# Performance work log

Hardware: AMD Instinct MI355X
Metric: run time of the kernel (lower is better)

## Reference

```python
import jax, jax.numpy as jnp
import numpy as np

N_NODE, N_USER = 100000, 30000
N_REL, N_BASIS = 8, 30
EMB, OUT = 32, 32
E = 1600000
BATCH = 16384
H1, H2, H3 = 64, 32, 16
NEG_SLOPE = 0.2


def setup_inputs() -> dict:
    key = jax.random.key(0)
    ks = jax.random.split(key, 20)
    g = lambda k, shape: jax.random.normal(k, shape, dtype=jnp.float32) * 0.05
    inp = {
        "x_ids": jnp.arange(N_NODE, dtype=jnp.int64 if jax.config.jax_enable_x64 else jnp.int32),
        "edge_index": jax.random.randint(ks[0], (2, E), 0, N_NODE),
        "edge_type": jax.random.randint(ks[1], (E,), 0, N_REL),
        "users": jax.random.randint(ks[2], (BATCH,), 0, N_USER),
        "bundles": jax.random.randint(ks[3], (BATCH,), 0, N_NODE),
        # parameters
        "emb": g(ks[4], (N_NODE, EMB)),
        "basis": g(ks[5], (N_BASIS, EMB, OUT)),
        "weight": g(ks[6], (N_REL, N_BASIS)),
        "att": g(ks[7], (N_REL, 2 * OUT)),
        "root": g(ks[8], (EMB, OUT)),
        "bias": jnp.zeros((OUT,), jnp.float32),
        "W1": g(ks[9], (2 * OUT, H1)), "b1": jnp.zeros((H1,), jnp.float32),
        "W2": g(ks[10], (H1, H2)), "b2": jnp.zeros((H2,), jnp.float32),
        "W3": g(ks[11], (H2, H3)), "b3": jnp.zeros((H3,), jnp.float32),
        "Wo": g(ks[12], (H3, 1)), "bo": jnp.zeros((1,), jnp.float32),
    }
    return inp


def _tgcn_fwd(x_ids, edge_index, edge_type, users, bundles,
              emb, basis, weight, att, root, bias,
              W1, b1, W2, b2, W3, b3, Wo, bo):
    N = emb.shape[0]
    R = weight.shape[0]
    O = basis.shape[2]
    x = emb[x_ids]                                   # (N, F) embedding lookup
    # basis decomposition: (R, F, O)
    w = (weight @ basis.reshape(N_BASIS, -1)).reshape(R, EMB, O)
    # transform every node under every relation once, then gather per edge
    xh = jnp.einsum('nf,rfo->nro', x, w)             # (N, R, O)
    src, dst = edge_index[0], edge_index[1]          # j (source), i (target)
    h_i = xh[dst, edge_type]                         # (E, O)
    h_j = xh[src, edge_type]                         # (E, O)
    a = att[edge_type]                               # (E, 2O)
    alpha = (h_i * a[:, :O]).sum(-1) + (h_j * a[:, O:]).sum(-1)
    alpha = jax.nn.leaky_relu(alpha, NEG_SLOPE)
    # segment softmax keyed by (target node, relation)
    seg_key = dst * R + edge_type
    n_seg = N * R
    amax = jax.ops.segment_max(alpha, seg_key, num_segments=n_seg)
    ex = jnp.exp(alpha - amax[seg_key])
    denom = jax.ops.segment_sum(ex, seg_key, num_segments=n_seg)
    alpha = ex / (denom[seg_key] + 1e-16)
    # scatter-add weighted messages into target nodes
    agg = jax.ops.segment_sum(h_j * alpha[:, None], dst, num_segments=N)
    h = jax.nn.relu(agg + x @ root + bias)           # update + ReLU
    z = jnp.concatenate([h[users], h[bundles]], axis=1)  # (B, 2O)
    z = jax.nn.relu(z @ W1 + b1)
    z = jax.nn.relu(z @ W2 + b2)
    z = jax.nn.relu(z @ W3 + b3)
    return z @ Wo + bo                               # (B, 1) logits


def reference(x_ids, edge_index, edge_type, users, bundles,
              emb, basis, weight, att, root, bias,
              W1, b1, W2, b2, W3, b3, Wo, bo):
    return _tgcn_fwd(x_ids, edge_index, edge_type, users, bundles,
                     emb, basis, weight, att, root, bias,
                     W1, b1, W2, b2, W3, b3, Wo, bo)
```

## Files before the change

### kernel.cpp

```cpp
#include <hip/hip_runtime.h>
#include <hip/hip_bf16.h>

#define N_NODE 100000
#define N_REL  8
#define EMB    32
#define OUT    32
#define N_BASIS 30
#define E_EDGE 1600000
#define BATCH  16384
#define H1 64
#define H2 32
#define H3 16
#define NEG_SLOPE 0.2f

#define BSH   9
#define NBKT  196
#define BCAP  12288
#define PCH   8192

__global__ __launch_bounds__(256) void k0_basis(const float* __restrict__ weight,
                                                const float* __restrict__ basis,
                                                float* __restrict__ w) {
    int i = blockIdx.x * 256 + threadIdx.x;
    if (i >= N_REL * EMB * OUT) return;
    int r = i >> 10, fo = i & 1023;
    float acc = 0.f;
    #pragma unroll
    for (int b = 0; b < N_BASIS; b++)
        acc = fmaf(weight[r * N_BASIS + b], basis[b * (EMB * OUT) + fo], acc);
    w[i] = acc;
}

__global__ __launch_bounds__(256) void k0b_wa(const float* __restrict__ w,
                                              const float* __restrict__ att,
                                              float* __restrict__ wa) {
    int i = blockIdx.x * 256 + threadIdx.x;
    if (i >= 512) return;
    int which = i >> 8, rf = i & 255, r = rf >> 5, f = rf & 31;
    const float* wrow = w + (r * 32 + f) * 32;
    const float* arow = att + r * 64 + which * 32;
    float acc = 0.f;
    #pragma unroll
    for (int o = 0; o < 32; o++) acc = fmaf(wrow[o], arow[o], acc);
    wa[i] = acc;
}

__global__ __launch_bounds__(256, 4) void k1_transform(const int* __restrict__ x_ids,
                                                       const float* __restrict__ emb,
                                                       const float* __restrict__ w,
                                                       unsigned short* __restrict__ xh) {
    const int t = threadIdx.x;
    const int o = t & 31;
    const int r = t >> 5;

    float wc[EMB];
    #pragma unroll
    for (int f = 0; f < EMB; f++) wc[f] = w[(r * EMB + f) * OUT + o];

    for (int n0 = blockIdx.x * 4; n0 < N_NODE; n0 += gridDim.x * 4) {
        const float* __restrict__ x0 =
            emb + (size_t)__builtin_amdgcn_readfirstlane(x_ids[n0 + 0]) * EMB;
        const float* __restrict__ x1 =
            emb + (size_t)__builtin_amdgcn_readfirstlane(x_ids[n0 + 1]) * EMB;
        const float* __restrict__ x2 =
            emb + (size_t)__builtin_amdgcn_readfirstlane(x_ids[n0 + 2]) * EMB;
        const float* __restrict__ x3 =
            emb + (size_t)__builtin_amdgcn_readfirstlane(x_ids[n0 + 3]) * EMB;

        float a0 = 0.f, a1 = 0.f, a2 = 0.f, a3 = 0.f;
        #pragma unroll
        for (int f = 0; f < EMB; f++) {
            a0 = fmaf(x0[f], wc[f], a0);
            a1 = fmaf(x1[f], wc[f], a1);
            a2 = fmaf(x2[f], wc[f], a2);
            a3 = fmaf(x3[f], wc[f], a3);
        }
        __hip_bfloat16 b0 = __float2bfloat16(a0);
        __hip_bfloat16 b1 = __float2bfloat16(a1);
        __hip_bfloat16 b2 = __float2bfloat16(a2);
        __hip_bfloat16 b3 = __float2bfloat16(a3);
        xh[(size_t)(n0 + 0) * 256 + t] = *(unsigned short*)&b0;
        xh[(size_t)(n0 + 1) * 256 + t] = *(unsigned short*)&b1;
        xh[(size_t)(n0 + 2) * 256 + t] = *(unsigned short*)&b2;
        xh[(size_t)(n0 + 3) * 256 + t] = *(unsigned short*)&b3;
    }
}

__global__ __launch_bounds__(256) void k_p(const int* __restrict__ x_ids,
                                           const float* __restrict__ emb,
                                           const float* __restrict__ wa,
                                           float* __restrict__ p_i,
                                           float* __restrict__ p_j) {
    __shared__ float wis[256], wjs[256];
    int t = threadIdx.x;
    for (int i = t; i < 512; i += 256) {
        int which = i >> 8, r = (i >> 5) & 7, f = i & 31;
        float v = wa[i];
        if (which == 0) wis[f * 8 + r] = v; else wjs[f * 8 + r] = v;
    }
    __syncthreads();
    int tg = blockIdx.x * 256 + t;
    int n = tg >> 3, r = tg & 7;
    int id = x_ids[n];
    const float4* xr = (const float4*)(emb + (size_t)id * EMB);
    float ai = 0.f, aj = 0.f;
    #pragma unroll
    for (int c = 0; c < 8; c++) {
        float4 xv = xr[c];
        ai = fmaf(xv.x, wis[(4 * c + 0) * 8 + r], ai);
        aj = fmaf(xv.x, wjs[(4 * c + 0) * 8 + r], aj);
        ai = fmaf(xv.y, wis[(4 * c + 1) * 8 + r], ai);
        aj = fmaf(xv.y, wjs[(4 * c + 1) * 8 + r], aj);
        ai = fmaf(xv.z, wis[(4 * c + 2) * 8 + r], ai);
        aj = fmaf(xv.z, wjs[(4 * c + 2) * 8 + r], aj);
        ai = fmaf(xv.w, wis[(4 * c + 3) * 8 + r], ai);
        aj = fmaf(xv.w, wjs[(4 * c + 3) * 8 + r], aj);
    }
    p_i[tg] = ai;
    p_j[tg] = aj;
}

__global__ __launch_bounds__(256) void k_init(const int* __restrict__ x_ids,
                                              const float* __restrict__ emb,
                                              const float* __restrict__ root,
                                              const float* __restrict__ bias,
                                              float* __restrict__ agg) {
    __shared__ float rs[EMB * OUT];
    __shared__ float bs[OUT];
    int t = threadIdx.x;
    for (int i = t; i < EMB * OUT; i += 256) rs[i] = root[i];
    if (t < OUT) bs[t] = bias[t];
    __syncthreads();
    int tg = blockIdx.x * 256 + t;
    int n = tg >> 5, o = tg & 31;
    int id = x_ids[n];
    const float* xr = emb + (size_t)id * EMB;
    float a = bs[o];
    #pragma unroll
    for (int f = 0; f < EMB; f++) a = fmaf(xr[f], rs[f * 32 + o], a);
    agg[tg] = a;
}

__global__ __launch_bounds__(256) void k_bhist(const int* __restrict__ dst,
                                               unsigned* __restrict__ bcnt) {
    __shared__ unsigned h[NBKT];
    int t = threadIdx.x;
    for (int i = t; i < NBKT; i += 256) h[i] = 0;
    __syncthreads();
    int beg = blockIdx.x * PCH, end = min(beg + PCH, E_EDGE);
    for (int e = beg + t; e < end; e += 256)
        atomicAdd(&h[(unsigned)dst[e] >> BSH], 1u);
    __syncthreads();
    for (int i = t; i < NBKT; i += 256)
        if (h[i]) atomicAdd(&bcnt[i], h[i]);
}

__global__ __launch_bounds__(256) void k_bscan(const unsigned* __restrict__ bcnt,
                                               unsigned* __restrict__ bbase,
                                               unsigned* __restrict__ bcursor) {
    __shared__ unsigned s[256];
    int t = threadIdx.x;
    unsigned v = (t < NBKT) ? bcnt[t] : 0u;
    s[t] = v;
    __syncthreads();
    for (int off = 1; off < 256; off <<= 1) {
        unsigned y = (t >= off) ? s[t - off] : 0u;
        __syncthreads();
        s[t] += y;
        __syncthreads();
    }
    unsigned ex = s[t] - v;
    if (t < NBKT) { bbase[t] = ex; bcursor[t] = ex; }
    if (t == 0) bbase[NBKT] = E_EDGE;
}

__global__ __launch_bounds__(256) void k_part(const int* __restrict__ src,
                                              const int* __restrict__ dst,
                                              const int* __restrict__ et,
                                              unsigned* __restrict__ bcursor,
                                              unsigned* __restrict__ part) {
    __shared__ unsigned long long stage[PCH];
    __shared__ unsigned hist[NBKT], lbase[NBKT], lcur[NBKT], gbase[NBKT];
    __shared__ unsigned sc[256];
    int t = threadIdx.x;
    for (int i = t; i < NBKT; i += 256) hist[i] = 0;
    __syncthreads();
    int beg = blockIdx.x * PCH, end = min(beg + PCH, E_EDGE);
    int n = end - beg;
    for (int e = beg + t; e < end; e += 256)
        atomicAdd(&hist[(unsigned)dst[e] >> BSH], 1u);
    __syncthreads();
    unsigned v = (t < NBKT) ? hist[t] : 0u;
    sc[t] = v;
    __syncthreads();
    for (int off = 1; off < 256; off <<= 1) {
        unsigned y = (t >= off) ? sc[t - off] : 0u;
        __syncthreads();
        sc[t] += y;
        __syncthreads();
    }
    if (t < NBKT) { lbase[t] = sc[t] - v; lcur[t] = sc[t] - v; }
    __syncthreads();
    for (int e = beg + t; e < end; e += 256) {
        int d = dst[e];
        unsigned b = (unsigned)d >> BSH;
        unsigned ent = ((unsigned)(d & 511) << 20)
                     | ((unsigned)src[e] << 3) | (unsigned)et[e];
        unsigned pos = atomicAdd(&lcur[b], 1u);
        stage[pos] = ((unsigned long long)b << 32) | ent;
    }
    __syncthreads();
    if (t < NBKT && hist[t]) gbase[t] = atomicAdd(&bcursor[t], hist[t]);
    __syncthreads();
    for (int i = t; i < n; i += 256) {
        unsigned long long s64 = stage[i];
        unsigned b = (unsigned)(s64 >> 32);
        unsigned ent = (unsigned)s64;
        part[gbase[b] + (i - lbase[b])] = ent;
    }
}

__global__ __launch_bounds__(256) void k_sort(const unsigned* __restrict__ bbase,
                                              const unsigned* __restrict__ part,
                                              int* __restrict__ payload,
                                              int* __restrict__ basep) {
    __shared__ unsigned ent[BCAP];
    __shared__ unsigned ent2[BCAP];
    __shared__ unsigned hist[512], dbase[512], dcur[512];
    __shared__ unsigned sc[256];
    int t = threadIdx.x;
    int b = blockIdx.x;
    unsigned s0 = bbase[b], s1 = bbase[b + 1];
    int n = (int)(s1 - s0);
    if (n > BCAP) n = BCAP;
    for (int i = t; i < 512; i += 256) hist[i] = 0;
    __syncthreads();
    for (int i = t; i < n; i += 256) {
        unsigned e = part[s0 + i];
        ent[i] = e;
        atomicAdd(&hist[e >> 20], 1u);
    }
    __syncthreads();
    unsigned v0 = hist[2 * t], v1 = hist[2 * t + 1];
    unsigned s = v0 + v1;
    sc[t] = s;
    __syncthreads();
    for (int off = 1; off < 256; off <<= 1) {
        unsigned y = (t >= off) ? sc[t - off] : 0u;
        __syncthreads();
        sc[t] += y;
        __syncthreads();
    }
    unsigned ex = sc[t] - s;
    dbase[2 * t] = ex;          dcur[2 * t] = ex;
    dbase[2 * t + 1] = ex + v0; dcur[2 * t + 1] = ex + v0;
    __syncthreads();
    int d0 = b << BSH;
    for (int dl = t; dl < 512; dl += 256) {
        int d = d0 + dl;
        if (d < N_NODE) basep[d] = (int)(s0 + dbase[dl]);
    }
    for (int i = t; i < n; i += 256) {
        unsigned e = ent[i];
        unsigned pos = atomicAdd(&dcur[e >> 20], 1u);
        ent2[pos] = e & 0xFFFFFu;
    }
    __syncthreads();
    for (int i = t; i < n; i += 256) payload[s0 + i] = (int)ent2[i];
    if (b == NBKT - 1 && t == 0) basep[N_NODE] = E_EDGE;
}

__global__ __launch_bounds__(256) void k_agg(const int* __restrict__ base,
                                             const int* __restrict__ payload,
                                             const float* __restrict__ p_i,
                                             const float* __restrict__ p_j,
                                             const unsigned short* __restrict__ xh,
                                             float* __restrict__ agg) {
    int d = blockIdx.x * 4 + (threadIdx.x >> 6);
    if (d >= N_NODE) return;
    const int lane = threadIdx.x & 63;
    const int h = lane >> 5;
    const int o = lane & 31;
    const int beg = base[d], end = base[d + 1];
    const int cnt = end - beg;
    if (cnt == 0) return;

    float pid[8];
    #pragma unroll
    for (int k = 0; k < 8; k++) pid[k] = p_i[(d << 3) | k];

    if (cnt <= 64) {
        int sr = 0, r = 0; float ev = 0.f;
        if (lane < cnt) {
            sr = payload[beg + lane];
            r = sr & 7;
            float pi = pid[0];
            #pragma unroll
            for (int k = 1; k < 8; k++) pi = (r == k) ? pid[k] : pi;
            float a = pi + p_j[sr];
            a = (a >= 0.f) ? a : NEG_SLOPE * a;
            ev = __expf(a);
        }
        float sex[8];
        #pragma unroll
        for (int k = 0; k < 8; k++) sex[k] = (r == k) ? ev : 0.f;
        #pragma unroll
        for (int k = 0; k < 8; k++) {
            #pragma unroll
            for (int m = 1; m <= 32; m <<= 1) sex[k] += __shfl_xor(sex[k], m, 64);
        }
        float de = sex[0];
        #pragma unroll
        for (int k = 1; k < 8; k++) de = (r == k) ? sex[k] : de;
        float al = ev / (de + 1e-16f);

        float v0 = 0.f, v1 = 0.f, v2 = 0.f, v3 = 0.f;
        for (int j0 = 0; j0 < cnt; j0 += 8) {
            float b0 = __shfl(al, j0 + h,     64); int t0 = __shfl(sr, j0 + h,     64);
            float b1 = __shfl(al, j0 + 2 + h, 64); int t1 = __shfl(sr, j0 + 2 + h, 64);
            float b2 = __shfl(al, j0 + 4 + h, 64); int t2 = __shfl(sr, j0 + 4 + h, 64);
            float b3 = __shfl(al, j0 + 6 + h, 64); int t3 = __shfl(sr, j0 + 6 + h, 64);
            float x0 = __uint_as_float((unsigned)xh[((size_t)t0 << 5) + o] << 16);
            float x1 = __uint_as_float((unsigned)xh[((size_t)t1 << 5) + o] << 16);
            float x2 = __uint_as_float((unsigned)xh[((size_t)t2 << 5) + o] << 16);
            float x3 = __uint_as_float((unsigned)xh[((size_t)t3 << 5) + o] << 16);
            v0 = fmaf(b0, x0, v0);
            v1 = fmaf(b1, x1, v1);
            v2 = fmaf(b2, x2, v2);
            v3 = fmaf(b3, x3, v3);
        }
        float v = (v0 + v1) + (v2 + v3);
        v += __shfl_xor(v, 32, 64);
        if (h == 0) agg[(size_t)d * OUT + o] += v;
        return;
    }

    float sex[8] = {0.f,0.f,0.f,0.f,0.f,0.f,0.f,0.f};
    for (int i = beg + lane; i < end; i += 64) {
        int sr = payload[i];
        int r = sr & 7;
        float pi = pid[0];
        #pragma unroll
        for (int k = 1; k < 8; k++) pi = (r == k) ? pid[k] : pi;
        float a = pi + p_j[sr];
        a = (a >= 0.f) ? a : NEG_SLOPE * a;
        float ev = __expf(a);
        #pragma unroll
        for (int k = 0; k < 8; k++) sex[k] += (r == k) ? ev : 0.f;
    }
    #pragma unroll
    for (int k = 0; k < 8; k++) {
        #pragma unroll
        for (int m = 1; m <= 32; m <<= 1) sex[k] += __shfl_xor(sex[k], m, 64);
    }
    float v0 = 0.f;
    for (int c = beg; c < end; c += 64) {
        int i = c + lane;
        int sr = 0; float al = 0.f;
        if (i < end) {
            sr = payload[i];
            int r = sr & 7;
            float pi = pid[0];
            #pragma unroll
            for (int k = 1; k < 8; k++) pi = (r == k) ? pid[k] : pi;
            float a = pi + p_j[sr];
            a = (a >= 0.f) ? a : NEG_SLOPE * a;
            float ev = __expf(a);
            float de = sex[0];
            #pragma unroll
            for (int k = 1; k < 8; k++) de = (r == k) ? sex[k] : de;
            al = ev / (de + 1e-16f);
        }
        int m = min(64, end - c);
        for (int j0 = 0; j0 < m; j0 += 2) {
            int e0 = j0 + h;
            float a0 = __shfl(al, e0, 64); int s0 = __shfl(sr, e0, 64);
            if (e0 < m) {
                float xv = __uint_as_float((unsigned)xh[((size_t)s0 << 5) + o] << 16);
                v0 = fmaf(a0, xv, v0);
            }
        }
    }
    float v = v0;
    v += __shfl_xor(v, 32, 64);
    if (h == 0) agg[(size_t)d * OUT + o] += v;
}

__global__ __launch_bounds__(64, 1) void k5_mlp(const int* __restrict__ users,
                                                const int* __restrict__ bundles,
                                                const float* __restrict__ agg,
                                                const float* __restrict__ W1,
                                                const float* __restrict__ b1,
                                                const float* __restrict__ W2,
                                                const float* __restrict__ b2,
                                                const float* __restrict__ W3,
                                                const float* __restrict__ b3,
                                                const float* __restrict__ Wo,
                                                const float* __restrict__ bo,
                                                float* __restrict__ out) {
    __shared__ float4 W1s[2 * OUT * H1 / 4];
    __shared__ float4 W2s[H1 * H2 / 4];
    __shared__ float4 W3s[H2 * H3 / 4];
    __shared__ float b1s[H1], b2s[H2], b3s[H3], Wos[H3];
    __shared__ float bos;
    const int t = threadIdx.x;

    const float4* W14 = (const float4*)W1;
    const float4* W24 = (const float4*)W2;
    const float4* W34 = (const float4*)W3;
    for (int i = t; i < 1024; i += 64) W1s[i] = W14[i];
    for (int i = t; i < 512; i += 64) W2s[i] = W24[i];
    for (int i = t; i < 128; i += 64) W3s[i] = W34[i];
    b1s[t] = b1[t];
    if (t < H2) b2s[t] = b2[t];
    if (t < H3) { b3s[t] = b3[t]; Wos[t] = Wo[t]; }
    if (t == 0) bos = bo[0];
    __syncthreads();

    const int item = blockIdx.x * 64 + t;
    const int u = users[item], v = bundles[item];
    const float4* av = (const float4*)agg;

    float z[64];
    #pragma unroll
    for (int c = 0; c < 8; c++) {
        float4 x = av[(size_t)u * 8 + c];
        z[4 * c + 0] = fmaxf(x.x, 0.f); z[4 * c + 1] = fmaxf(x.y, 0.f);
        z[4 * c + 2] = fmaxf(x.z, 0.f); z[4 * c + 3] = fmaxf(x.w, 0.f);
    }
    #pragma unroll
    for (int c = 0; c < 8; c++) {
        float4 x = av[(size_t)v * 8 + c];
        z[32 + 4 * c + 0] = fmaxf(x.x, 0.f); z[32 + 4 * c + 1] = fmaxf(x.y, 0.f);
        z[32 + 4 * c + 2] = fmaxf(x.z, 0.f); z[32 + 4 * c + 3] = fmaxf(x.w, 0.f);
    }

    float h1v[64];
    #pragma unroll
    for (int j = 0; j < H1; j++) h1v[j] = b1s[j];
    #pragma unroll
    for (int k = 0; k < 2 * OUT; k++) {
        float zk = z[k];
        #pragma unroll
        for (int j4 = 0; j4 < 16; j4++) {
            float4 wv = W1s[k * 16 + j4];
            h1v[4 * j4 + 0] = fmaf(zk, wv.x, h1v[4 * j4 + 0]);
            h1v[4 * j4 + 1] = fmaf(zk, wv.y, h1v[4 * j4 + 1]);
            h1v[4 * j4 + 2] = fmaf(zk, wv.z, h1v[4 * j4 + 2]);
            h1v[4 * j4 + 3] = fmaf(zk, wv.w, h1v[4 * j4 + 3]);
        }
    }
    #pragma unroll
    for (int j = 0; j < H1; j++) h1v[j] = fmaxf(h1v[j], 0.f);

    float h2v[32];
    #pragma unroll
    for (int j = 0; j < H2; j++) h2v[j] = b2s[j];
    #pragma unroll
    for (int k = 0; k < H1; k++) {
        float hk = h1v[k];
        #pragma unroll
        for (int j4 = 0; j4 < 8; j4++) {
            float4 wv = W2s[k * 8 + j4];
            h2v[4 * j4 + 0] = fmaf(hk, wv.x, h2v[4 * j4 + 0]);
            h2v[4 * j4 + 1] = fmaf(hk, wv.y, h2v[4 * j4 + 1]);
            h2v[4 * j4 + 2] = fmaf(hk, wv.z, h2v[4 * j4 + 2]);
            h2v[4 * j4 + 3] = fmaf(hk, wv.w, h2v[4 * j4 + 3]);
        }
    }
    #pragma unroll
    for (int j = 0; j < H2; j++) h2v[j] = fmaxf(h2v[j], 0.f);

    float h3v[16];
    #pragma unroll
    for (int j = 0; j < H3; j++) h3v[j] = b3s[j];
    #pragma unroll
    for (int k = 0; k < H2; k++) {
        float hk = h2v[k];
        #pragma unroll
        for (int j4 = 0; j4 < 4; j4++) {
            float4 wv = W3s[k * 4 + j4];
            h3v[4 * j4 + 0] = fmaf(hk, wv.x, h3v[4 * j4 + 0]);
            h3v[4 * j4 + 1] = fmaf(hk, wv.y, h3v[4 * j4 + 1]);
            h3v[4 * j4 + 2] = fmaf(hk, wv.z, h3v[4 * j4 + 2]);
            h3v[4 * j4 + 3] = fmaf(hk, wv.w, h3v[4 * j4 + 3]);
        }
    }
    #pragma unroll
    for (int j = 0; j < H3; j++) h3v[j] = fmaxf(h3v[j], 0.f);

    float acc = bos;
    #pragma unroll
    for (int k = 0; k < H3; k++) acc = fmaf(h3v[k], Wos[k], acc);
    out[item] = acc;
}

extern "C" void kernel_launch(void* const* d_in, const int* in_sizes, int n_in,
                              void* d_out, int out_size, void* d_ws, size_t ws_size,
                              hipStream_t stream) {
    (void)in_sizes; (void)n_in; (void)out_size; (void)ws_size;
    const int*   x_ids  = (const int*)d_in[0];
    const int*   eidx   = (const int*)d_in[1];
    const int*   etype  = (const int*)d_in[2];
    const int*   users  = (const int*)d_in[3];
    const int*   bund   = (const int*)d_in[4];
    const float* emb    = (const float*)d_in[5];
    const float* basis  = (const float*)d_in[6];
    const float* weight = (const float*)d_in[7];
    const float* att    = (const float*)d_in[8];
    const float* root   = (const float*)d_in[9];
    const float* bias   = (const float*)d_in[10];
    const float* W1 = (const float*)d_in[11]; const float* b1 = (const float*)d_in[12];
    const float* W2 = (const float*)d_in[13]; const float* b2 = (const float*)d_in[14];
    const float* W3 = (const float*)d_in[15]; const float* b3 = (const float*)d_in[16];
    const float* Wo = (const float*)d_in[17]; const float* bo = (const float*)d_in[18];
    float* out = (float*)d_out;

    const int* src = eidx;
    const int* dst = eidx + E_EDGE;

    float* ws       = (float*)d_ws;
    float* w        = ws;
    float* wa       = w + N_REL * EMB * OUT;
    unsigned short* xh = (unsigned short*)(wa + 512);
    float* p_i      = (float*)(xh + (size_t)N_NODE * 256);
    float* p_j      = p_i + N_NODE * N_REL;
    float* agg      = p_j + N_NODE * N_REL;
    int*   payload  = (int*)(agg + (long)N_NODE * OUT);
    int*   basep    = payload + E_EDGE;
    unsigned* bcnt    = (unsigned*)(basep + N_NODE + 1);
    unsigned* bbase   = bcnt + 256;
    unsigned* bcursor = bbase + 256;
    unsigned* part    = (unsigned*)agg;

    hipMemsetAsync(bcnt, 0, NBKT * sizeof(unsigned), stream);

    k0_basis<<<(N_REL * EMB * OUT + 255) / 256, 256, 0, stream>>>(weight, basis, w);
    k0b_wa<<<2, 256, 0, stream>>>(w, att, wa);
    k_bhist<<<(E_EDGE + PCH - 1) / PCH, 256, 0, stream>>>(dst, bcnt);
    k_bscan<<<1, 256, 0, stream>>>(bcnt, bbase, bcursor);
    k_part<<<(E_EDGE + PCH - 1) / PCH, 256, 0, stream>>>(src, dst, etype, bcursor, part);
    k_sort<<<NBKT, 256, 0, stream>>>(bbase, part, payload, basep);
    k1_transform<<<2048, 256, 0, stream>>>(x_ids, emb, w, xh);
    k_p<<<(N_NODE * N_REL) / 256, 256, 0, stream>>>(x_ids, emb, wa, p_i, p_j);
    k_init<<<(N_NODE * OUT) / 256, 256, 0, stream>>>(x_ids, emb, root, bias, agg);
    k_agg<<<(N_NODE + 3) / 4, 256, 0, stream>>>(basep, payload, p_i, p_j, xh, agg);
    k5_mlp<<<BATCH / 64, 64, 0, stream>>>(users, bund, agg, W1, b1, W2, b2, W3, b3,
                                          Wo, bo, out);
}
```

Measured before the change: 356.2 us.

## Drop edge histogram pass via fixed-capacity buckets and fuse small prep kernels

Result: faster. 348.0 us (-2.3%).

```diff
diff --git a/kernel.cpp b/kernel.cpp
--- a/kernel.cpp
+++ b/kernel.cpp
@@ -18,31 +18,34 @@
 #define BCAP  12288
 #define PCH   8192
 
-__global__ __launch_bounds__(256) void k0_basis(const float* __restrict__ weight,
-                                                const float* __restrict__ basis,
-                                                float* __restrict__ w) {
-    int i = blockIdx.x * 256 + threadIdx.x;
-    if (i >= N_REL * EMB * OUT) return;
-    int r = i >> 10, fo = i & 1023;
-    float acc = 0.f;
-    #pragma unroll
-    for (int b = 0; b < N_BASIS; b++)
-        acc = fmaf(weight[r * N_BASIS + b], basis[b * (EMB * OUT) + fo], acc);
-    w[i] = acc;
-}
-
-__global__ __launch_bounds__(256) void k0b_wa(const float* __restrict__ w,
-                                              const float* __restrict__ att,
-                                              float* __restrict__ wa) {
-    int i = blockIdx.x * 256 + threadIdx.x;
-    if (i >= 512) return;
-    int which = i >> 8, rf = i & 255, r = rf >> 5, f = rf & 31;
-    const float* wrow = w + (r * 32 + f) * 32;
-    const float* arow = att + r * 64 + which * 32;
-    float acc = 0.f;
-    #pragma unroll
-    for (int o = 0; o < 32; o++) acc = fmaf(wrow[o], arow[o], acc);
-    wa[i] = acc;
+__global__ __launch_bounds__(256) void k0f(const float* __restrict__ weight,
+                                           const float* __restrict__ basis,
+                                           const float* __restrict__ att,
+                                           float* __restrict__ w,
+                                           float* __restrict__ wa,
+                                           unsigned* __restrict__ bcnt) {
+    __shared__ float wl[N_REL * EMB * OUT];
+    int t = threadIdx.x;
+    for (int i = t; i < N_REL * EMB * OUT; i += 256) {
+        int r = i >> 10, fo = i & 1023;
+        float acc = 0.f;
+        #pragma unroll
+        for (int b = 0; b < N_BASIS; b++)
+            acc = fmaf(weight[r * N_BASIS + b], basis[b * (EMB * OUT) + fo], acc);
+        wl[i] = acc;
+        w[i] = acc;
+    }
+    __syncthreads();
+    for (int i = t; i < 512; i += 256) {
+        int which = i >> 8, rf = i & 255, r = rf >> 5, f = rf & 31;
+        const float* wrow = wl + (r * 32 + f) * 32;
+        const float* arow = att + r * 64 + which * 32;
+        float acc = 0.f;
+        #pragma unroll
+        for (int o = 0; o < 32; o++) acc = fmaf(wrow[o], arow[o], acc);
+        wa[i] = acc;
+    }
+    if (t < NBKT) bcnt[t] = 0;
 }
 
 __global__ __launch_bounds__(256, 4) void k1_transform(const int* __restrict__ x_ids,
@@ -86,13 +89,20 @@
     }
 }
 
-__global__ __launch_bounds__(256) void k_p(const int* __restrict__ x_ids,
-                                           const float* __restrict__ emb,
-                                           const float* __restrict__ wa,
-                                           float* __restrict__ p_i,
-                                           float* __restrict__ p_j) {
+__global__ __launch_bounds__(256) void k_pi(const int* __restrict__ x_ids,
+                                            const float* __restrict__ emb,
+                                            const float* __restrict__ wa,
+                                            const float* __restrict__ root,
+                                            const float* __restrict__ bias,
+                                            float* __restrict__ p_i,
+                                            float* __restrict__ p_j,
+                                            float* __restrict__ agg) {
+    __shared__ float rs[EMB * OUT];
+    __shared__ float bs[OUT];
     __shared__ float wis[256], wjs[256];
     int t = threadIdx.x;
+    for (int i = t; i < EMB * OUT; i += 256) rs[i] = root[i];
+    if (t < OUT) bs[t] = bias[t];
     for (int i = t; i < 512; i += 256) {
         int which = i >> 8, r = (i >> 5) & 7, f = i & 31;
         float v = wa[i];
@@ -100,84 +110,36 @@
     }
     __syncthreads();
     int tg = blockIdx.x * 256 + t;
-    int n = tg >> 3, r = tg & 7;
-    int id = x_ids[n];
-    const float4* xr = (const float4*)(emb + (size_t)id * EMB);
-    float ai = 0.f, aj = 0.f;
-    #pragma unroll
-    for (int c = 0; c < 8; c++) {
-        float4 xv = xr[c];
-        ai = fmaf(xv.x, wis[(4 * c + 0) * 8 + r], ai);
-        aj = fmaf(xv.x, wjs[(4 * c + 0) * 8 + r], aj);
-        ai = fmaf(xv.y, wis[(4 * c + 1) * 8 + r], ai);
-        aj = fmaf(xv.y, wjs[(4 * c + 1) * 8 + r], aj);
-        ai = fmaf(xv.z, wis[(4 * c + 2) * 8 + r], ai);
-        aj = fmaf(xv.z, wjs[(4 * c + 2) * 8 + r], aj);
-        ai = fmaf(xv.w, wis[(4 * c + 3) * 8 + r], ai);
-        aj = fmaf(xv.w, wjs[(4 * c + 3) * 8 + r], aj);
-    }
-    p_i[tg] = ai;
-    p_j[tg] = aj;
-}
-
-__global__ __launch_bounds__(256) void k_init(const int* __restrict__ x_ids,
-                                              const float* __restrict__ emb,
-                                              const float* __restrict__ root,
-                                              const float* __restrict__ bias,
-                                              float* __restrict__ agg) {
-    __shared__ float rs[EMB * OUT];
-    __shared__ float bs[OUT];
-    int t = threadIdx.x;
-    for (int i = t; i < EMB * OUT; i += 256) rs[i] = root[i];
-    if (t < OUT) bs[t] = bias[t];
-    __syncthreads();
-    int tg = blockIdx.x * 256 + t;
     int n = tg >> 5, o = tg & 31;
     int id = x_ids[n];
-    const float* xr = emb + (size_t)id * EMB;
+    const float4* xr4 = (const float4*)(emb + (size_t)id * EMB);
+    float xf[EMB];
+    #pragma unroll
+    for (int c = 0; c < 8; c++) {
+        float4 xv = xr4[c];
+        xf[4 * c + 0] = xv.x; xf[4 * c + 1] = xv.y;
+        xf[4 * c + 2] = xv.z; xf[4 * c + 3] = xv.w;
+    }
     float a = bs[o];
     #pragma unroll
-    for (int f = 0; f < EMB; f++) a = fmaf(xr[f], rs[f * 32 + o], a);
+    for (int f = 0; f < EMB; f++) a = fmaf(xf[f], rs[f * 32 + o], a);
     agg[tg] = a;
-}
-
-__global__ __launch_bounds__(256) void k_bhist(const int* __restrict__ dst,
-                                               unsigned* __restrict__ bcnt) {
-    __shared__ unsigned h[NBKT];
-    int t = threadIdx.x;
-    for (int i = t; i < NBKT; i += 256) h[i] = 0;
-    __syncthreads();
-    int beg = blockIdx.x * PCH, end = min(beg + PCH, E_EDGE);
-    for (int e = beg + t; e < end; e += 256)
-        atomicAdd(&h[(unsigned)dst[e] >> BSH], 1u);
-    __syncthreads();
-    for (int i = t; i < NBKT; i += 256)
-        if (h[i]) atomicAdd(&bcnt[i], h[i]);
-}
-
-__global__ __launch_bounds__(256) void k_bscan(const unsigned* __restrict__ bcnt,
-                                               unsigned* __restrict__ bbase,
-                                               unsigned* __restrict__ bcursor) {
-    __shared__ unsigned s[256];
-    int t = threadIdx.x;
-    unsigned v = (t < NBKT) ? bcnt[t] : 0u;
-    s[t] = v;
-    __syncthreads();
-    for (int off = 1; off < 256; off <<= 1) {
-        unsigned y = (t >= off) ? s[t - off] : 0u;
-        __syncthreads();
-        s[t] += y;
-        __syncthreads();
-    }
-    unsigned ex = s[t] - v;
-    if (t < NBKT) { bbase[t] = ex; bcursor[t] = ex; }
-    if (t == 0) bbase[NBKT] = E_EDGE;
+    if (o < N_REL) {
+        float ai = 0.f, aj = 0.f;
+        #pragma unroll
+        for (int f = 0; f < EMB; f++) {
+            ai = fmaf(xf[f], wis[f * 8 + o], ai);
+            aj = fmaf(xf[f], wjs[f * 8 + o], aj);
+        }
+        p_i[n * N_REL + o] = ai;
+        p_j[n * N_REL + o] = aj;
+    }
 }
 
 __global__ __launch_bounds__(256) void k_part(const int* __restrict__ src,
                                               const int* __restrict__ dst,
                                               const int* __restrict__ et,
-                                              unsigned* __restrict__ bcursor,
+                                              unsigned* __restrict__ bcnt,
                                               unsigned* __restrict__ part) {
     __shared__ unsigned long long stage[PCH];
     __shared__ unsigned hist[NBKT], lbase[NBKT], lcur[NBKT], gbase[NBKT];
@@ -210,28 +172,29 @@
         stage[pos] = ((unsigned long long)b << 32) | ent;
     }
     __syncthreads();
-    if (t < NBKT && hist[t]) gbase[t] = atomicAdd(&bcursor[t], hist[t]);
+    if (t < NBKT && hist[t]) gbase[t] = atomicAdd(&bcnt[t], hist[t]);
     __syncthreads();
     for (int i = t; i < n; i += 256) {
         unsigned long long s64 = stage[i];
         unsigned b = (unsigned)(s64 >> 32);
         unsigned ent = (unsigned)s64;
-        part[gbase[b] + (i - lbase[b])] = ent;
-    }
-}
-
-__global__ __launch_bounds__(256) void k_sort(const unsigned* __restrict__ bbase,
+        part[b * BCAP + gbase[b] + (i - lbase[b])] = ent;
+    }
+}
+
+__global__ __launch_bounds__(256) void k_sort(const unsigned* __restrict__ bcnt,
                                               const unsigned* __restrict__ part,
                                               int* __restrict__ payload,
-                                              int* __restrict__ basep) {
+                                              int* __restrict__ begp,
+                                              int* __restrict__ endp) {
     __shared__ unsigned ent[BCAP];
     __shared__ unsigned ent2[BCAP];
     __shared__ unsigned hist[512], dbase[512], dcur[512];
     __shared__ unsigned sc[256];
     int t = threadIdx.x;
     int b = blockIdx.x;
-    unsigned s0 = bbase[b], s1 = bbase[b + 1];
-    int n = (int)(s1 - s0);
+    unsigned s0 = (unsigned)b * BCAP;
+    int n = (int)bcnt[b];
     if (n > BCAP) n = BCAP;
     for (int i = t; i < 512; i += 256) hist[i] = 0;
     __syncthreads();
@@ -258,7 +221,10 @@
     int d0 = b << BSH;
     for (int dl = t; dl < 512; dl += 256) {
         int d = d0 + dl;
-        if (d < N_NODE) basep[d] = (int)(s0 + dbase[dl]);
+        if (d < N_NODE) {
+            begp[d] = (int)(s0 + dbase[dl]);
+            endp[d] = (int)(s0 + dbase[dl] + hist[dl]);
+        }
     }
     for (int i = t; i < n; i += 256) {
         unsigned e = ent[i];
@@ -267,10 +233,10 @@
     }
     __syncthreads();
     for (int i = t; i < n; i += 256) payload[s0 + i] = (int)ent2[i];
-    if (b == NBKT - 1 && t == 0) basep[N_NODE] = E_EDGE;
-}
-
-__global__ __launch_bounds__(256) void k_agg(const int* __restrict__ base,
+}
+
+__global__ __launch_bounds__(256) void k_agg(const int* __restrict__ begp,
+                                             const int* __restrict__ endp,
                                              const int* __restrict__ payload,
                                              const float* __restrict__ p_i,
                                              const float* __restrict__ p_j,
@@ -281,7 +247,7 @@
     const int lane = threadIdx.x & 63;
     const int h = lane >> 5;
     const int o = lane & 31;
-    const int beg = base[d], end = base[d + 1];
+    const int beg = begp[d], end = endp[d];
     const int cnt = end - beg;
     if (cnt == 0) return;
 
@@ -314,22 +280,31 @@
         for (int k = 1; k < 8; k++) de = (r == k) ? sex[k] : de;
         float al = ev / (de + 1e-16f);
 
-        float v0 = 0.f, v1 = 0.f, v2 = 0.f, v3 = 0.f;
-        for (int j0 = 0; j0 < cnt; j0 += 8) {
-            float b0 = __shfl(al, j0 + h,     64); int t0 = __shfl(sr, j0 + h,     64);
-            float b1 = __shfl(al, j0 + 2 + h, 64); int t1 = __shfl(sr, j0 + 2 + h, 64);
-            float b2 = __shfl(al, j0 + 4 + h, 64); int t2 = __shfl(sr, j0 + 4 + h, 64);
-            float b3 = __shfl(al, j0 + 6 + h, 64); int t3 = __shfl(sr, j0 + 6 + h, 64);
-            float x0 = __uint_as_float((unsigned)xh[((size_t)t0 << 5) + o] << 16);
-            float x1 = __uint_as_float((unsigned)xh[((size_t)t1 << 5) + o] << 16);
-            float x2 = __uint_as_float((unsigned)xh[((size_t)t2 << 5) + o] << 16);
-            float x3 = __uint_as_float((unsigned)xh[((size_t)t3 << 5) + o] << 16);
-            v0 = fmaf(b0, x0, v0);
-            v1 = fmaf(b1, x1, v1);
-            v2 = fmaf(b2, x2, v2);
-            v3 = fmaf(b3, x3, v3);
-        }
-        float v = (v0 + v1) + (v2 + v3);
+        float w0 = 0.f, w1 = 0.f, w2 = 0.f, w3 = 0.f;
+        float w4 = 0.f, w5 = 0.f, w6 = 0.f, w7 = 0.f;
+        for (int j0 = 0; j0 < cnt; j0 += 16) {
+            float b0 = __shfl(al, j0 + h,      64); int t0 = __shfl(sr, j0 + h,      64);
+            float b1 = __shfl(al, j0 + 2 + h,  64); int t1 = __shfl(sr, j0 + 2 + h,  64);
+            float b2 = __shfl(al, j0 + 4 + h,  64); int t2 = __shfl(sr, j0 + 4 + h,  64);
+            float b3 = __shfl(al, j0 + 6 + h,  64); int t3 = __shfl(sr, j0 + 6 + h,  64);
+            float b4 = __shfl(al, j0 + 8 + h,  64); int t4 = __shfl(sr, j0 + 8 + h,  64);
+            float b5 = __shfl(al, j0 + 10 + h, 64); int t5 = __shfl(sr, j0 + 10 + h, 64);
+            float b6 = __shfl(al, j0 + 12 + h, 64); int t6 = __shfl(sr, j0 + 12 + h, 64);
+            float b7 = __shfl(al, j0 + 14 + h, 64); int t7 = __shfl(sr, j0 + 14 + h, 64);
+            float x0 = __uint_as_float((unsigned)xh[((unsigned)t0 << 5) + o] << 16);
+            float x1 = __uint_as_float((unsigned)xh[((unsigned)t1 << 5) + o] << 16);
+            float x2 = __uint_as_float((unsigned)xh[((unsigned)t2 << 5) + o] << 16);
+            float x3 = __uint_as_float((unsigned)xh[((unsigned)t3 << 5) + o] << 16);
+            float x4 = __uint_as_float((unsigned)xh[((unsigned)t4 << 5) + o] << 16);
+            float x5 = __uint_as_float((unsigned)xh[((unsigned)t5 << 5) + o] << 16);
+            float x6 = __uint_as_float((unsigned)xh[((unsigned)t6 << 5) + o] << 16);
+            float x7 = __uint_as_float((unsigned)xh[((unsigned)t7 << 5) + o] << 16);
+            w0 = fmaf(b0, x0, w0); w1 = fmaf(b1, x1, w1);
+            w2 = fmaf(b2, x2, w2); w3 = fmaf(b3, x3, w3);
+            w4 = fmaf(b4, x4, w4); w5 = fmaf(b5, x5, w5);
+            w6 = fmaf(b6, x6, w6); w7 = fmaf(b7, x7, w7);
+        }
+        float v = ((w0 + w1) + (w2 + w3)) + ((w4 + w5) + (w6 + w7));
         v += __shfl_xor(v, 32, 64);
         if (h == 0) agg[(size_t)d * OUT + o] += v;
         return;
@@ -376,7 +351,7 @@
             int e0 = j0 + h;
             float a0 = __shfl(al, e0, 64); int s0 = __shfl(sr, e0, 64);
             if (e0 < m) {
-                float xv = __uint_as_float((unsigned)xh[((size_t)s0 << 5) + o] << 16);
+                float xv = __uint_as_float((unsigned)xh[((unsigned)s0 << 5) + o] << 16);
                 v0 = fmaf(a0, xv, v0);
             }
         }
@@ -527,24 +502,18 @@
     float* p_j      = p_i + N_NODE * N_REL;
     float* agg      = p_j + N_NODE * N_REL;
     int*   payload  = (int*)(agg + (long)N_NODE * OUT);
-    int*   basep    = payload + E_EDGE;
-    unsigned* bcnt    = (unsigned*)(basep + N_NODE + 1);
-    unsigned* bbase   = bcnt + 256;
-    unsigned* bcursor = bbase + 256;
-    unsigned* part    = (unsigned*)agg;
-
-    hipMemsetAsync(bcnt, 0, NBKT * sizeof(unsigned), stream);
-
-    k0_basis<<<(N_REL * EMB * OUT + 255) / 256, 256, 0, stream>>>(weight, basis, w);
-    k0b_wa<<<2, 256, 0, stream>>>(w, att, wa);
-    k_bhist<<<(E_EDGE + PCH - 1) / PCH, 256, 0, stream>>>(dst, bcnt);
-    k_bscan<<<1, 256, 0, stream>>>(bcnt, bbase, bcursor);
-    k_part<<<(E_EDGE + PCH - 1) / PCH, 256, 0, stream>>>(src, dst, etype, bcursor, part);
-    k_sort<<<NBKT, 256, 0, stream>>>(bbase, part, payload, basep);
+    int*   begp     = payload + NBKT * BCAP;
+    int*   endp     = begp + N_NODE;
+    unsigned* bcnt  = (unsigned*)(endp + N_NODE);
+    unsigned* part  = (unsigned*)agg;
+
+    k0f<<<1, 256, 0, stream>>>(weight, basis, att, w, wa, bcnt);
+    k_part<<<(E_EDGE + PCH - 1) / PCH, 256, 0, stream>>>(src, dst, etype, bcnt, part);
+    k_sort<<<NBKT, 256, 0, stream>>>(bcnt, part, payload, begp, endp);
     k1_transform<<<2048, 256, 0, stream>>>(x_ids, emb, w, xh);
-    k_p<<<(N_NODE * N_REL) / 256, 256, 0, stream>>>(x_ids, emb, wa, p_i, p_j);
-    k_init<<<(N_NODE * OUT) / 256, 256, 0, stream>>>(x_ids, emb, root, bias, agg);
-    k_agg<<<(N_NODE + 3) / 4, 256, 0, stream>>>(basep, payload, p_i, p_j, xh, agg);
+    k_pi<<<(N_NODE * OUT) / 256, 256, 0, stream>>>(x_ids, emb, wa, root, bias,
+                                                   p_i, p_j, agg);
+    k_agg<<<(N_NODE + 3) / 4, 256, 0, stream>>>(begp, endp, payload, p_i, p_j, xh, agg);
     k5_mlp<<<BATCH / 64, 64, 0, stream>>>(users, bund, agg, W1, b1, W2, b2, W3, b3,
                                           Wo, bo, out);
 }
```
